# Performance work log

Measured on AMD Instinct MI355X. Metric: run time of the kernel, lower is better.

## Reference

```python
import jax, jax.numpy as jnp
import numpy as np

IN_F = 4096
OUT_F = 4096
Q_LEVELS = 16  # 4-bit


def setup_inputs() -> dict:
    key = jax.random.key(0)
    k = jax.random.split(key, 7)
    input = jax.random.normal(k[0], (4, 128, IN_F), dtype=jnp.float32)
    qweight = jax.random.randint(k[1], (OUT_F, IN_F), 0, Q_LEVELS, dtype=jnp.int32)
    scales = jax.random.uniform(k[2], (OUT_F, 1), dtype=jnp.float32)
    zeros = jax.random.uniform(k[3], (OUT_F, 1), dtype=jnp.float32)
    outlier = jax.random.uniform(k[4], (OUT_F, IN_F), dtype=jnp.float32)
    grad_updates = jax.random.normal(k[5], (OUT_F, IN_F), dtype=jnp.float32)
    bias = jax.random.normal(k[6], (OUT_F,), dtype=jnp.float32)
    return {"input": input, "qweight": qweight, "scales": scales,
            "zeros": zeros, "outlier": outlier,
            "grad_updates": grad_updates, "bias": bias}


def reference(input, qweight, scales, zeros, outlier, grad_updates, bias):
    # dequantize: affine per-output-row quantization -> dense weight [out, in]
    weight = (qweight.astype(jnp.float32) - zeros) * scales
    # sparse outlier correction (densified), scaled by learned GradUpdates
    weight = weight + outlier * grad_updates
    # F.linear: y = x @ W^T + b
    return jnp.einsum('bsi,oi->bso', input, weight) + bias
```

## Files before the change

### kernel.cpp

```cpp
#include <hip/hip_runtime.h>
#include <stdint.h>

#define IN_F   4096
#define OUT_F  4096
#define M_TOT  512
#define KT     (IN_F / 32)
#define BN     64
#define BK     64
#define KSPLIT 4
#define KPB    (IN_F / KSPLIT)
#define NITER  (KPB / BK)

typedef unsigned short u16;
typedef __bf16 bf16x8 __attribute__((ext_vector_type(8)));
typedef float  f32x4  __attribute__((ext_vector_type(4)));
typedef int    i32x4  __attribute__((ext_vector_type(4)));
typedef float  fv4    __attribute__((ext_vector_type(4)));

__device__ __forceinline__ u16 f2bf(float x) {
    unsigned u = __float_as_uint(x);
    u += 0x7FFFu + ((u >> 16) & 1u);
    return (u16)(u >> 16);
}

__global__ void pack_a_kernel(const float* __restrict__ in, u16* __restrict__ aws) {
    int t    = blockIdx.x * blockDim.x + threadIdx.x;
    int lane = t & 63;
    int kt   = (t >> 6) & (KT - 1);
    int mt   = t >> 13;
    int m = mt * 16 + (lane & 15);
    int k = kt * 32 + ((lane >> 4) << 3);
    const float* src = in + (size_t)m * IN_F + k;
    float4 a0 = *(const float4*)src;
    float4 a1 = *(const float4*)(src + 4);
    union { u16 u[8]; uint4 v; } pk;
    pk.u[0]=f2bf(a0.x); pk.u[1]=f2bf(a0.y); pk.u[2]=f2bf(a0.z); pk.u[3]=f2bf(a0.w);
    pk.u[4]=f2bf(a1.x); pk.u[5]=f2bf(a1.y); pk.u[6]=f2bf(a1.z); pk.u[7]=f2bf(a1.w);
    *(uint4*)(aws + (size_t)t * 8) = pk.v;
}

__global__ __launch_bounds__(1024, 4) void qlinear_kernel(
    const u16*   __restrict__ aws,
    const int*   __restrict__ qw,
    const float* __restrict__ scales,
    const float* __restrict__ zeros,
    const float* __restrict__ outlier,
    const float* __restrict__ grad,
    float*       __restrict__ part)
{
    __shared__ __align__(16) u16 Bsh[2][8 * 64 * 8];

    const int tid  = threadIdx.x;
    const int lane = tid & 63;
    const int wv   = tid >> 6;

    const int nblk = blockIdx.x >> 2;
    const int kq   = blockIdx.x & 3;
    const int n0   = nblk * BN;
    const int k0   = kq * KPB;

    const int srow = tid >> 4;
    const int schk = tid & 15;
    const int orow = n0 + srow;
    const float sr = scales[orow];
    const float c0 = -zeros[orow] * sr;
    const size_t sg = (size_t)orow * IN_F + k0 + schk * 4;
    const int sks   = schk >> 3;
    const int squad = (schk >> 1) & 3;
    const int j0    = (schk & 1) * 4;
    const int snf   = srow >> 4;
    const int slane = (srow & 15) | (squad << 4);
    const int doff  = ((sks * 4 + snf) * 64 + slane) * 8 + j0;

    i32x4 qb[2]; fv4 ob[2], gb[2];
    auto ld = [&](int it) {
        int s = it & 1;
        size_t off = sg + (size_t)it * BK;
        qb[s] = __builtin_nontemporal_load((const i32x4*)(qw      + off));
        ob[s] = __builtin_nontemporal_load((const fv4*)  (outlier + off));
        gb[s] = __builtin_nontemporal_load((const fv4*)  (grad    + off));
    };
    auto st = [&](int it) {
        int s = it & 1;
        union { u16 u[4]; uint2 v; } pk;
        pk.u[0] = f2bf(fmaf((float)qb[s].x, sr, fmaf(ob[s].x, gb[s].x, c0)));
        pk.u[1] = f2bf(fmaf((float)qb[s].y, sr, fmaf(ob[s].y, gb[s].y, c0)));
        pk.u[2] = f2bf(fmaf((float)qb[s].z, sr, fmaf(ob[s].z, gb[s].z, c0)));
        pk.u[3] = f2bf(fmaf((float)qb[s].w, sr, fmaf(ob[s].w, gb[s].w, c0)));
        *(uint2*)(&Bsh[it & 1][doff]) = pk.v;
    };

    const u16* abase = aws + ((size_t)(wv * 2) * KT + kq * (KPB / 32)) * 512
                           + (size_t)lane * 8;

    f32x4 acc[2][4] = {};

    ld(0);
    st(0);
    ld(1);
    __syncthreads();

    for (int it = 0; it < NITER; ++it) {
        bf16x8 af[2][2];
        #pragma unroll
        for (int ks = 0; ks < 2; ++ks)
            #pragma unroll
            for (int mf = 0; mf < 2; ++mf)
                af[ks][mf] = *(const bf16x8*)(abase + ((size_t)mf * KT + it * 2 + ks) * 512);

        const u16* bb = &Bsh[it & 1][0];
        #pragma unroll
        for (int ks = 0; ks < 2; ++ks) {
            bf16x8 bfr[4];
            #pragma unroll
            for (int nf = 0; nf < 4; ++nf)
                bfr[nf] = *(const bf16x8*)(bb + (((ks * 4 + nf) * 64) + lane) * 8);
            #pragma unroll
            for (int mf = 0; mf < 2; ++mf)
                #pragma unroll
                for (int nf = 0; nf < 4; ++nf)
                    acc[mf][nf] = __builtin_amdgcn_mfma_f32_16x16x32_bf16(
                        af[ks][mf], bfr[nf], acc[mf][nf], 0, 0, 0);
        }

        if (it + 1 < NITER) st(it + 1);
        if (it + 2 < NITER) ld(it + 2);
        __syncthreads();
    }

    float* pout = part + (size_t)kq * (M_TOT * OUT_F);
    const int cm0 = wv * 32 + ((lane >> 4) << 2);
    const int cn  = n0 + (lane & 15);
    #pragma unroll
    for (int mf = 0; mf < 2; ++mf)
        #pragma unroll
        for (int nf = 0; nf < 4; ++nf)
            #pragma unroll
            for (int r = 0; r < 4; ++r)
                __builtin_nontemporal_store(
                    acc[mf][nf][r],
                    pout + (size_t)(cm0 + mf * 16 + r) * OUT_F + cn + nf * 16);
}

__global__ void reduce_kernel(const fv4* __restrict__ part,
                              const fv4* __restrict__ bias,
                              fv4* __restrict__ out) {
    int idx = blockIdx.x * blockDim.x + threadIdx.x;
    fv4 s = bias[idx & (OUT_F / 4 - 1)];
    const int STRIDE = M_TOT * OUT_F / 4;
    #pragma unroll
    for (int k = 0; k < KSPLIT; ++k) {
        fv4 p = __builtin_nontemporal_load(part + (size_t)k * STRIDE + idx);
        s += p;
    }
    out[idx] = s;
}

extern "C" void kernel_launch(void* const* d_in, const int* in_sizes, int n_in,
                              void* d_out, int out_size, void* d_ws, size_t ws_size,
                              hipStream_t stream) {
    const float* input   = (const float*)d_in[0];
    const int*   qweight = (const int*)  d_in[1];
    const float* scales  = (const float*)d_in[2];
    const float* zeros   = (const float*)d_in[3];
    const float* outlier = (const float*)d_in[4];
    const float* grad    = (const float*)d_in[5];
    const float* bias    = (const float*)d_in[6];
    float* out = (float*)d_out;

    u16*   aws  = (u16*)d_ws;
    float* part = (float*)((char*)d_ws + (4u << 20));

    pack_a_kernel<<<(M_TOT * IN_F / 8) / 256, 256, 0, stream>>>(input, aws);
    qlinear_kernel<<<(OUT_F / BN) * KSPLIT, 1024, 0, stream>>>(
        aws, qweight, scales, zeros, outlier, grad, part);
    reduce_kernel<<<(M_TOT * OUT_F / 4) / 256, 256, 0, stream>>>(
        (const fv4*)part, (const fv4*)bias, (fv4*)out);
}
```

Before: 219.0 us.

## Replace split-K partial buffers and reduce kernel with atomic adds into output

Drops the 4-way partial-sum buffer and the separate reduce kernel. The output is zeroed in the pack kernel and each K-split block atomically adds its tile, with the bias added only by the kq==0 block. Inside the GEMM loop, the global prefetch and the LDS store of the next tile now happen before the MFMAs, so they overlap with compute. The nontemporal hints on the weight loads are also removed. This saves about 32 MB of partial-buffer traffic and one launch, at the cost of atomic contention and a float summation order that is no longer deterministic.

```diff
diff --git a/kernel.cpp b/kernel.cpp
--- a/kernel.cpp
+++ b/kernel.cpp
@@ -23,7 +23,8 @@
     return (u16)(u >> 16);
 }
 
-__global__ void pack_a_kernel(const float* __restrict__ in, u16* __restrict__ aws) {
+__global__ void pack_a_kernel(const float* __restrict__ in, u16* __restrict__ aws,
+                              float* __restrict__ outz) {
     int t    = blockIdx.x * blockDim.x + threadIdx.x;
     int lane = t & 63;
     int kt   = (t >> 6) & (KT - 1);
@@ -37,6 +38,9 @@
     pk.u[0]=f2bf(a0.x); pk.u[1]=f2bf(a0.y); pk.u[2]=f2bf(a0.z); pk.u[3]=f2bf(a0.w);
     pk.u[4]=f2bf(a1.x); pk.u[5]=f2bf(a1.y); pk.u[6]=f2bf(a1.z); pk.u[7]=f2bf(a1.w);
     *(uint4*)(aws + (size_t)t * 8) = pk.v;
+    f32x4 z = {};
+    ((f32x4*)outz)[t] = z;
+    ((f32x4*)outz)[t + (M_TOT * OUT_F / 8)] = z;
 }
 
 __global__ __launch_bounds__(1024, 4) void qlinear_kernel(
@@ -46,7 +50,8 @@
     const float* __restrict__ zeros,
     const float* __restrict__ outlier,
     const float* __restrict__ grad,
-    float*       __restrict__ part)
+    const float* __restrict__ bias,
+    float*       __restrict__ out)
 {
     __shared__ __align__(16) u16 Bsh[2][8 * 64 * 8];
 
@@ -76,9 +81,9 @@
     auto ld = [&](int it) {
         int s = it & 1;
         size_t off = sg + (size_t)it * BK;
-        qb[s] = __builtin_nontemporal_load((const i32x4*)(qw      + off));
-        ob[s] = __builtin_nontemporal_load((const fv4*)  (outlier + off));
-        gb[s] = __builtin_nontemporal_load((const fv4*)  (grad    + off));
+        qb[s] = *(const i32x4*)(qw      + off);
+        ob[s] = *(const fv4*)  (outlier + off);
+        gb[s] = *(const fv4*)  (grad    + off);
     };
     auto st = [&](int it) {
         int s = it & 1;
@@ -101,12 +106,16 @@
     __syncthreads();
 
     for (int it = 0; it < NITER; ++it) {
+        if (it + 2 < NITER) ld(it + 2);
+
         bf16x8 af[2][2];
         #pragma unroll
         for (int ks = 0; ks < 2; ++ks)
             #pragma unroll
             for (int mf = 0; mf < 2; ++mf)
                 af[ks][mf] = *(const bf16x8*)(abase + ((size_t)mf * KT + it * 2 + ks) * 512);
+
+        if (it + 1 < NITER) st(it + 1);
 
         const u16* bb = &Bsh[it & 1][0];
         #pragma unroll
@@ -123,37 +132,23 @@
                         af[ks][mf], bfr[nf], acc[mf][nf], 0, 0, 0);
         }
 
-        if (it + 1 < NITER) st(it + 1);
-        if (it + 2 < NITER) ld(it + 2);
         __syncthreads();
     }
 
-    float* pout = part + (size_t)kq * (M_TOT * OUT_F);
     const int cm0 = wv * 32 + ((lane >> 4) << 2);
     const int cn  = n0 + (lane & 15);
+    float badd[4];
+    #pragma unroll
+    for (int nf = 0; nf < 4; ++nf)
+        badd[nf] = (kq == 0) ? bias[cn + nf * 16] : 0.0f;
     #pragma unroll
     for (int mf = 0; mf < 2; ++mf)
         #pragma unroll
         for (int nf = 0; nf < 4; ++nf)
             #pragma unroll
             for (int r = 0; r < 4; ++r)
-                __builtin_nontemporal_store(
-                    acc[mf][nf][r],
-                    pout + (size_t)(cm0 + mf * 16 + r) * OUT_F + cn + nf * 16);
-}
-
-__global__ void reduce_kernel(const fv4* __restrict__ part,
-                              const fv4* __restrict__ bias,
-                              fv4* __restrict__ out) {
-    int idx = blockIdx.x * blockDim.x + threadIdx.x;
-    fv4 s = bias[idx & (OUT_F / 4 - 1)];
-    const int STRIDE = M_TOT * OUT_F / 4;
-    #pragma unroll
-    for (int k = 0; k < KSPLIT; ++k) {
-        fv4 p = __builtin_nontemporal_load(part + (size_t)k * STRIDE + idx);
-        s += p;
-    }
-    out[idx] = s;
+                unsafeAtomicAdd(out + (size_t)(cm0 + mf * 16 + r) * OUT_F + cn + nf * 16,
+                                acc[mf][nf][r] + badd[nf]);
 }
 
 extern "C" void kernel_launch(void* const* d_in, const int* in_sizes, int n_in,
@@ -168,12 +163,9 @@
     const float* bias    = (const float*)d_in[6];
     float* out = (float*)d_out;
 
-    u16*   aws  = (u16*)d_ws;
-    float* part = (float*)((char*)d_ws + (4u << 20));
+    u16* aws = (u16*)d_ws;
 
-    pack_a_kernel<<<(M_TOT * IN_F / 8) / 256, 256, 0, stream>>>(input, aws);
+    pack_a_kernel<<<(M_TOT * IN_F / 8) / 256, 256, 0, stream>>>(input, aws, out);
     qlinear_kernel<<<(OUT_F / BN) * KSPLIT, 1024, 0, stream>>>(
-        aws, qweight, scales, zeros, outlier, grad, part);
-    reduce_kernel<<<(M_TOT * OUT_F / 4) / 256, 256, 0, stream>>>(
-        (const fv4*)part, (const fv4*)bias, (fv4*)out);
+        aws, qweight, scales, zeros, outlier, grad, bias, out);
 }
```

New measurement: 250.9 us. 1.15x slower.

## Narrow N tile to 32, widen K tile to 128, single-stage register prefetch

Applied to the files above, without the earlier changes.

Halves the output-column tile per block and doubles the K step, so each thread dequantizes 4 elements covering a 32x128 weight slab per iteration, and the grid has twice as many blocks. The two-deep register prefetch becomes a single prefetch issued at the top of each iteration. Nontemporal loads of the weight streams become plain loads, and A fragments are loaded inside the ks loop. The intent is more blocks for memory parallelism and more occupancy, since launch bounds rise to 8 per CU. The cost is that A reuse per block falls, because each A fragment now feeds only two N fragments.

```diff
diff --git a/kernel.cpp b/kernel.cpp
--- a/kernel.cpp
+++ b/kernel.cpp
@@ -5,8 +5,8 @@
 #define OUT_F  4096
 #define M_TOT  512
 #define KT     (IN_F / 32)
-#define BN     64
-#define BK     64
+#define BN     32
+#define BK     128
 #define KSPLIT 4
 #define KPB    (IN_F / KSPLIT)
 #define NITER  (KPB / BK)
@@ -39,7 +39,7 @@
     *(uint4*)(aws + (size_t)t * 8) = pk.v;
 }
 
-__global__ __launch_bounds__(1024, 4) void qlinear_kernel(
+__global__ __launch_bounds__(1024, 8) void qlinear_kernel(
     const u16*   __restrict__ aws,
     const int*   __restrict__ qw,
     const float* __restrict__ scales,
@@ -59,8 +59,8 @@
     const int n0   = nblk * BN;
     const int k0   = kq * KPB;
 
-    const int srow = tid >> 4;
-    const int schk = tid & 15;
+    const int srow = tid >> 5;
+    const int schk = tid & 31;
     const int orow = n0 + srow;
     const float sr = scales[orow];
     const float c0 = -zeros[orow] * sr;
@@ -70,61 +70,51 @@
     const int j0    = (schk & 1) * 4;
     const int snf   = srow >> 4;
     const int slane = (srow & 15) | (squad << 4);
-    const int doff  = ((sks * 4 + snf) * 64 + slane) * 8 + j0;
+    const int doff  = ((sks * 2 + snf) * 64 + slane) * 8 + j0;
 
-    i32x4 qb[2]; fv4 ob[2], gb[2];
+    i32x4 qb; fv4 ob, gb;
     auto ld = [&](int it) {
-        int s = it & 1;
         size_t off = sg + (size_t)it * BK;
-        qb[s] = __builtin_nontemporal_load((const i32x4*)(qw      + off));
-        ob[s] = __builtin_nontemporal_load((const fv4*)  (outlier + off));
-        gb[s] = __builtin_nontemporal_load((const fv4*)  (grad    + off));
+        qb = *(const i32x4*)(qw      + off);
+        ob = *(const fv4*)  (outlier + off);
+        gb = *(const fv4*)  (grad    + off);
     };
     auto st = [&](int it) {
-        int s = it & 1;
         union { u16 u[4]; uint2 v; } pk;
-        pk.u[0] = f2bf(fmaf((float)qb[s].x, sr, fmaf(ob[s].x, gb[s].x, c0)));
-        pk.u[1] = f2bf(fmaf((float)qb[s].y, sr, fmaf(ob[s].y, gb[s].y, c0)));
-        pk.u[2] = f2bf(fmaf((float)qb[s].z, sr, fmaf(ob[s].z, gb[s].z, c0)));
-        pk.u[3] = f2bf(fmaf((float)qb[s].w, sr, fmaf(ob[s].w, gb[s].w, c0)));
+        pk.u[0] = f2bf(fmaf((float)qb.x, sr, fmaf(ob.x, gb.x, c0)));
+        pk.u[1] = f2bf(fmaf((float)qb.y, sr, fmaf(ob.y, gb.y, c0)));
+        pk.u[2] = f2bf(fmaf((float)qb.z, sr, fmaf(ob.z, gb.z, c0)));
+        pk.u[3] = f2bf(fmaf((float)qb.w, sr, fmaf(ob.w, gb.w, c0)));
         *(uint2*)(&Bsh[it & 1][doff]) = pk.v;
     };
 
     const u16* abase = aws + ((size_t)(wv * 2) * KT + kq * (KPB / 32)) * 512
                            + (size_t)lane * 8;
 
-    f32x4 acc[2][4] = {};
+    f32x4 acc[2][2] = {};
 
     ld(0);
     st(0);
-    ld(1);
     __syncthreads();
 
     for (int it = 0; it < NITER; ++it) {
-        bf16x8 af[2][2];
-        #pragma unroll
-        for (int ks = 0; ks < 2; ++ks)
-            #pragma unroll
-            for (int mf = 0; mf < 2; ++mf)
-                af[ks][mf] = *(const bf16x8*)(abase + ((size_t)mf * KT + it * 2 + ks) * 512);
+        if (it + 1 < NITER) ld(it + 1);
 
         const u16* bb = &Bsh[it & 1][0];
+        const u16* ab = abase + (size_t)(it * 4) * 512;
         #pragma unroll
-        for (int ks = 0; ks < 2; ++ks) {
-            bf16x8 bfr[4];
-            #pragma unroll
-            for (int nf = 0; nf < 4; ++nf)
-                bfr[nf] = *(const bf16x8*)(bb + (((ks * 4 + nf) * 64) + lane) * 8);
-            #pragma unroll
-            for (int mf = 0; mf < 2; ++mf)
-                #pragma unroll
-                for (int nf = 0; nf < 4; ++nf)
-                    acc[mf][nf] = __builtin_amdgcn_mfma_f32_16x16x32_bf16(
-                        af[ks][mf], bfr[nf], acc[mf][nf], 0, 0, 0);
+        for (int ks = 0; ks < 4; ++ks) {
+            bf16x8 af0 = *(const bf16x8*)(ab + (size_t)ks * 512);
+            bf16x8 af1 = *(const bf16x8*)(ab + ((size_t)KT + ks) * 512);
+            bf16x8 bf0 = *(const bf16x8*)(bb + (((ks * 2 + 0) * 64) + lane) * 8);
+            bf16x8 bf1 = *(const bf16x8*)(bb + (((ks * 2 + 1) * 64) + lane) * 8);
+            acc[0][0] = __builtin_amdgcn_mfma_f32_16x16x32_bf16(af0, bf0, acc[0][0], 0, 0, 0);
+            acc[0][1] = __builtin_amdgcn_mfma_f32_16x16x32_bf16(af0, bf1, acc[0][1], 0, 0, 0);
+            acc[1][0] = __builtin_amdgcn_mfma_f32_16x16x32_bf16(af1, bf0, acc[1][0], 0, 0, 0);
+            acc[1][1] = __builtin_amdgcn_mfma_f32_16x16x32_bf16(af1, bf1, acc[1][1], 0, 0, 0);
         }
 
         if (it + 1 < NITER) st(it + 1);
-        if (it + 2 < NITER) ld(it + 2);
         __syncthreads();
     }
 
@@ -134,7 +124,7 @@
     #pragma unroll
     for (int mf = 0; mf < 2; ++mf)
         #pragma unroll
-        for (int nf = 0; nf < 4; ++nf)
+        for (int nf = 0; nf < 2; ++nf)
             #pragma unroll
             for (int r = 0; r < 4; ++r)
                 __builtin_nontemporal_store(
```

Result: slower. 233.4 us (+6.6%).
